# Kernel optimization log

Hardware: AMD Instinct MI355X
Metric: run time of the kernel (lower is better)

Reference implementation:

```python
import jax, jax.numpy as jnp
import numpy as np

B, H, W, C = 32, 512, 512, 3
OUT_H, OUT_W = 224, 224


def setup_inputs() -> dict:
    key = jax.random.key(0)
    k1, k2 = jax.random.split(key)
    images = jax.random.uniform(k1, (B, H, W, C), dtype=jnp.float32)
    identity = jnp.array([[1.0, 0.0, 0.0], [0.0, 1.0, 0.0]], dtype=jnp.float32)
    matrices = identity[None] + 0.05 * jax.random.normal(k2, (B, 2, 3), dtype=jnp.float32)
    return {"images": images, "matrices": matrices}


def _affine_warp(image, M):
    # image: (H, W, C); M: (2, 3) mapping output pixel (y, x, 1) -> source (y, x).
    h, w, _ = image.shape
    dt = image.dtype
    ys, xs = jnp.meshgrid(jnp.arange(h, dtype=dt), jnp.arange(w, dtype=dt), indexing="ij")
    src_y = M[0, 0] * ys + M[0, 1] * xs + M[0, 2]
    src_x = M[1, 0] * ys + M[1, 1] * xs + M[1, 2]
    y0 = jnp.floor(src_y)
    x0 = jnp.floor(src_x)
    wy = (src_y - y0)[..., None]
    wx = (src_x - x0)[..., None]
    y0i = y0.astype(jnp.int32)
    x0i = x0.astype(jnp.int32)

    def gather(yi, xi):
        valid = (yi >= 0) & (yi < h) & (xi >= 0) & (xi < w)
        yc = jnp.clip(yi, 0, h - 1)
        xc = jnp.clip(xi, 0, w - 1)
        return image[yc, xc] * valid[..., None].astype(dt)  # zero fill outside

    v00 = gather(y0i, x0i)
    v01 = gather(y0i, x0i + 1)
    v10 = gather(y0i + 1, x0i)
    v11 = gather(y0i + 1, x0i + 1)
    top = v00 * (1.0 - wx) + v01 * wx
    bot = v10 * (1.0 - wx) + v11 * wx
    return top * (1.0 - wy) + bot * wy


def reference(images, matrices):
    # batch_transform: per-sample affine warp (bilinear sampling, zero padding)
    warped = jax.vmap(_affine_warp)(images, matrices)  # (B, H, W, C)
    # batch_resize: bilinear resize to the layer's target shape
    b, _, _, c = warped.shape
    return jax.image.resize(warped, (b, OUT_H, OUT_W, c), method="bilinear")
```

## Files before the change

kernel.cpp:

```cpp
#include <hip/hip_runtime.h>
#include <hip/hip_bf16.h>
#include <math.h>

constexpr int B  = 32;
constexpr int H  = 512;
constexpr int W  = 512;
constexpr int OH = 224;
constexpr int OW = 224;

constexpr int TILE = 16;
constexpr int WIN  = 40;
constexpr int NT   = OH / TILE;
constexpr int NB   = B * NT * NT;
constexpr int THREADS = 256;

__global__ __launch_bounds__(THREADS, 8) void warp_resize_tiled(const float* __restrict__ img,
                                                                const float* __restrict__ mats,
                                                                float* __restrict__ out) {
    __shared__ __hip_bfloat16 sWp[3][WIN][WIN];
    __shared__ float          sV[TILE][WIN * 3];

    int bid = (int)blockIdx.x;
    bid = (bid & 7) * (NB / 8) + (bid >> 3);

    const int b   = bid / (NT * NT);
    const int rm  = bid % (NT * NT);
    const int ty  = rm / NT;
    const int tx  = rm % NT;
    const int tid = (int)threadIdx.x;

    const float* Mp = mats + b * 6;
    const float m00 = Mp[0], m01 = Mp[1], m02 = Mp[2];
    const float m10 = Mp[3], m11 = Mp[4], m12 = Mp[5];

    const float s     = 512.0f / 224.0f;
    const float invks = 224.0f / 512.0f;

    const int oy_base = ty * TILE;
    const int ox_base = tx * TILE;
    const int jy0 = (int)ceilf((oy_base + 0.5f) * s - 0.5f - s);
    const int jx0 = (int)ceilf((ox_base + 0.5f) * s - 0.5f - s);

    const float* imgb = img + (size_t)b * H * W * 3;

    const float y_lo = (float)jy0, y_hi = (float)(jy0 + WIN - 1);
    const float x_lo = (float)jx0, x_hi = (float)(jx0 + WIN - 1);
    const float cy00 = m00 * y_lo + m01 * x_lo + m02;
    const float cy01 = m00 * y_lo + m01 * x_hi + m02;
    const float cy10 = m00 * y_hi + m01 * x_lo + m02;
    const float cy11 = m00 * y_hi + m01 * x_hi + m02;
    const float cx00 = m10 * y_lo + m11 * x_lo + m12;
    const float cx01 = m10 * y_lo + m11 * x_hi + m12;
    const float cx10 = m10 * y_hi + m11 * x_lo + m12;
    const float cx11 = m10 * y_hi + m11 * x_hi + m12;
    const float miny = fminf(fminf(cy00, cy01), fminf(cy10, cy11));
    const float maxy = fmaxf(fmaxf(cy00, cy01), fmaxf(cy10, cy11));
    const float minx = fminf(fminf(cx00, cx01), fminf(cx10, cx11));
    const float maxx = fmaxf(fmaxf(cx00, cx01), fmaxf(cx10, cx11));
    const bool interior = (miny >= 0.01f) && (maxy <= 510.9f) &&
                          (minx >= 0.01f) && (maxx <= 510.9f);

    if (interior) {
        for (int e = tid; e < WIN * WIN; e += THREADS) {
            const int r = e / WIN;
            const int c = e - r * WIN;
            const float yf = (float)(jy0 + r);
            const float xf = (float)(jx0 + c);
            const float src_y = m00 * yf + m01 * xf + m02;
            const float src_x = m10 * yf + m11 * xf + m12;
            const float fy0 = floorf(src_y);
            const float fx0 = floorf(src_x);
            const float fy  = src_y - fy0;
            const float fx  = src_x - fx0;
            const int off = ((int)fy0 * W + (int)fx0) * 3;
            const float* p0 = imgb + off;
            const float* p1 = p0 + W * 3;
            const float a0 = p0[0], a1 = p0[1], a2 = p0[2];
            const float a3 = p0[3], a4 = p0[4], a5 = p0[5];
            const float b0 = p1[0], b1 = p1[1], b2 = p1[2];
            const float b3 = p1[3], b4 = p1[4], b5 = p1[5];
            const float w00 = (1.0f - fy) * (1.0f - fx);
            const float w01 = (1.0f - fy) * fx;
            const float w10 = fy * (1.0f - fx);
            const float w11 = fy * fx;
            sWp[0][r][c] = __float2bfloat16(a0 * w00 + a3 * w01 + b0 * w10 + b3 * w11);
            sWp[1][r][c] = __float2bfloat16(a1 * w00 + a4 * w01 + b1 * w10 + b4 * w11);
            sWp[2][r][c] = __float2bfloat16(a2 * w00 + a5 * w01 + b2 * w10 + b5 * w11);
        }
    } else {
        for (int e = tid; e < WIN * WIN; e += THREADS) {
            const int r = e / WIN;
            const int c = e - r * WIN;
            const float yf = (float)(jy0 + r);
            const float xf = (float)(jx0 + c);
            const float src_y = m00 * yf + m01 * xf + m02;
            const float src_x = m10 * yf + m11 * xf + m12;
            const float fy0 = floorf(src_y);
            const float fx0 = floorf(src_x);
            const float fy  = src_y - fy0;
            const float fx  = src_x - fx0;
            const int iy0 = (int)fy0;
            const int ix0 = (int)fx0;
            float v[4][3];
#pragma unroll
            for (int t = 0; t < 4; ++t) {
                const int yi = iy0 + (t >> 1);
                const int xi = ix0 + (t & 1);
                if (yi >= 0 && yi < H && xi >= 0 && xi < W) {
                    const float* p = imgb + (yi * W + xi) * 3;
                    v[t][0] = p[0]; v[t][1] = p[1]; v[t][2] = p[2];
                } else {
                    v[t][0] = 0.0f; v[t][1] = 0.0f; v[t][2] = 0.0f;
                }
            }
            const float w00 = (1.0f - fy) * (1.0f - fx);
            const float w01 = (1.0f - fy) * fx;
            const float w10 = fy * (1.0f - fx);
            const float w11 = fy * fx;
            sWp[0][r][c] = __float2bfloat16(v[0][0] * w00 + v[1][0] * w01 + v[2][0] * w10 + v[3][0] * w11);
            sWp[1][r][c] = __float2bfloat16(v[0][1] * w00 + v[1][1] * w01 + v[2][1] * w10 + v[3][1] * w11);
            sWp[2][r][c] = __float2bfloat16(v[0][2] * w00 + v[1][2] * w01 + v[2][2] * w10 + v[3][2] * w11);
        }
    }
    __syncthreads();

    for (int e = tid; e < TILE * WIN; e += THREADS) {
        const int r = e / WIN;
        const int c = e - r * WIN;
        const int oy = oy_base + r;
        const float sfy = (oy + 0.5f) * s - 0.5f;
        const int j0 = (int)ceilf(sfy - s);
        float wk[5];
        float sum = 0.0f;
#pragma unroll
        for (int k = 0; k < 5; ++k) {
            const int jy = j0 + k;
            float wv = 1.0f - fabsf(sfy - (float)jy) * invks;
            wv = (jy >= 0 && jy < H) ? fmaxf(wv, 0.0f) : 0.0f;
            wk[k] = wv; sum += wv;
        }
        const float inv = 1.0f / sum;
        float a0 = 0.0f, a1 = 0.0f, a2 = 0.0f;
#pragma unroll
        for (int k = 0; k < 5; ++k) {
            const int rr = j0 + k - jy0;
            const float wv = wk[k];
            a0 += wv * __bfloat162float(sWp[0][rr][c]);
            a1 += wv * __bfloat162float(sWp[1][rr][c]);
            a2 += wv * __bfloat162float(sWp[2][rr][c]);
        }
        sV[r][c * 3 + 0] = a0 * inv;
        sV[r][c * 3 + 1] = a1 * inv;
        sV[r][c * 3 + 2] = a2 * inv;
    }
    __syncthreads();

    {
        const int oxl = tid % TILE;
        const int oyl = tid / TILE;
        const int ox  = ox_base + oxl;
        const int oy  = oy_base + oyl;
        const float sfx = (ox + 0.5f) * s - 0.5f;
        const int j0 = (int)ceilf(sfx - s);
        float wk[5];
        float sum = 0.0f;
#pragma unroll
        for (int k = 0; k < 5; ++k) {
            const int jx = j0 + k;
            float wv = 1.0f - fabsf(sfx - (float)jx) * invks;
            wv = (jx >= 0 && jx < W) ? fmaxf(wv, 0.0f) : 0.0f;
            wk[k] = wv; sum += wv;
        }
        const float inv = 1.0f / sum;
        float a0 = 0.0f, a1 = 0.0f, a2 = 0.0f;
#pragma unroll
        for (int k = 0; k < 5; ++k) {
            const int cc = j0 + k - jx0;
            const float wv = wk[k];
            a0 += wv * sV[oyl][cc * 3 + 0];
            a1 += wv * sV[oyl][cc * 3 + 1];
            a2 += wv * sV[oyl][cc * 3 + 2];
        }
        float* o = out + (((size_t)b * OH + oy) * OW + ox) * 3;
        o[0] = a0 * inv;
        o[1] = a1 * inv;
        o[2] = a2 * inv;
    }
}

extern "C" void kernel_launch(void* const* d_in, const int* in_sizes, int n_in,
                              void* d_out, int out_size, void* d_ws, size_t ws_size,
                              hipStream_t stream) {
    const float* img  = (const float*)d_in[0];
    const float* mats = (const float*)d_in[1];
    float*       out  = (float*)d_out;

    hipLaunchKernelGGL(warp_resize_tiled, dim3(NB), dim3(THREADS), 0, stream, img, mats, out);
}
```

Baseline: 161.1 us.

## Pack bf16 channels into uint2 in shared memory and precompute resize weights

Stores the three warped channels per pixel as packed bf16 in a single uint2 shared-memory entry, so one 8-byte LDS replaces three separate 2-byte loads. The intermediate vertical-pass buffer also becomes packed bf16 instead of fp32. Per-row and per-column resize weights are computed once by 32 threads into shared tables with normalization folded in, instead of being recomputed in every inner loop. This cuts LDS instruction count and ALU work, but adds another bf16 rounding step on the intermediate, which reduces accuracy.

```diff
diff --git a/kernel.cpp b/kernel.cpp
--- a/kernel.cpp
+++ b/kernel.cpp
@@ -14,11 +14,26 @@
 constexpr int NB   = B * NT * NT;
 constexpr int THREADS = 256;
 
+union BfPack { __hip_bfloat162 h; unsigned u; };
+
+static __device__ inline unsigned pack_bf2(float a, float b) {
+    BfPack p; p.h = __float22bfloat162_rn(make_float2(a, b));
+    return p.u;
+}
+static __device__ inline unsigned pack_bf1(float a) {
+    BfPack p; p.h = __float22bfloat162_rn(make_float2(a, 0.0f));
+    return p.u;
+}
+static __device__ inline float lo_bf(unsigned q) { return __uint_as_float(q << 16); }
+static __device__ inline float hi_bf(unsigned q) { return __uint_as_float(q & 0xffff0000u); }
+
 __global__ __launch_bounds__(THREADS, 8) void warp_resize_tiled(const float* __restrict__ img,
                                                                 const float* __restrict__ mats,
                                                                 float* __restrict__ out) {
-    __shared__ __hip_bfloat16 sWp[3][WIN][WIN];
-    __shared__ float          sV[TILE][WIN * 3];
+    __shared__ uint2 sW[WIN][WIN];
+    __shared__ uint2 sV[TILE][WIN];
+    __shared__ float wyt[TILE][5], wxt[TILE][5];
+    __shared__ int   jyt[TILE], jxt[TILE];
 
     int bid = (int)blockIdx.x;
     bid = (bid & 7) * (NB / 8) + (bid >> 3);
@@ -42,6 +57,33 @@
     const int jx0 = (int)ceilf((ox_base + 0.5f) * s - 0.5f - s);
 
     const float* imgb = img + (size_t)b * H * W * 3;
+
+    if (tid < 2 * TILE) {
+        const bool isx = tid >= TILE;
+        const int  i   = isx ? tid - TILE : tid;
+        const int  ob  = isx ? ox_base : oy_base;
+        const int  jw0 = isx ? jx0 : jy0;
+        const float sf = ((float)(ob + i) + 0.5f) * s - 0.5f;
+        const int  j0 = (int)ceilf(sf - s);
+        float w[5]; float sum = 0.0f;
+#pragma unroll
+        for (int k = 0; k < 5; ++k) {
+            const int j = j0 + k;
+            float wv = 1.0f - fabsf(sf - (float)j) * invks;
+            wv = (j >= 0 && j < H) ? fmaxf(wv, 0.0f) : 0.0f;
+            w[k] = wv; sum += wv;
+        }
+        const float inv = 1.0f / sum;
+        if (isx) {
+            jxt[i] = j0 - jw0;
+#pragma unroll
+            for (int k = 0; k < 5; ++k) wxt[i][k] = w[k] * inv;
+        } else {
+            jyt[i] = j0 - jw0;
+#pragma unroll
+            for (int k = 0; k < 5; ++k) wyt[i][k] = w[k] * inv;
+        }
+    }
 
     const float y_lo = (float)jy0, y_hi = (float)(jy0 + WIN - 1);
     const float x_lo = (float)jx0, x_hi = (float)(jx0 + WIN - 1);
@@ -83,9 +125,11 @@
             const float w01 = (1.0f - fy) * fx;
             const float w10 = fy * (1.0f - fx);
             const float w11 = fy * fx;
-            sWp[0][r][c] = __float2bfloat16(a0 * w00 + a3 * w01 + b0 * w10 + b3 * w11);
-            sWp[1][r][c] = __float2bfloat16(a1 * w00 + a4 * w01 + b1 * w10 + b4 * w11);
-            sWp[2][r][c] = __float2bfloat16(a2 * w00 + a5 * w01 + b2 * w10 + b5 * w11);
+            const float c0 = a0 * w00 + a3 * w01 + b0 * w10 + b3 * w11;
+            const float c1 = a1 * w00 + a4 * w01 + b1 * w10 + b4 * w11;
+            const float c2 = a2 * w00 + a5 * w01 + b2 * w10 + b5 * w11;
+            uint2 q; q.x = pack_bf2(c0, c1); q.y = pack_bf1(c2);
+            sW[r][c] = q;
         }
     } else {
         for (int e = tid; e < WIN * WIN; e += THREADS) {
@@ -117,9 +161,11 @@
             const float w01 = (1.0f - fy) * fx;
             const float w10 = fy * (1.0f - fx);
             const float w11 = fy * fx;
-            sWp[0][r][c] = __float2bfloat16(v[0][0] * w00 + v[1][0] * w01 + v[2][0] * w10 + v[3][0] * w11);
-            sWp[1][r][c] = __float2bfloat16(v[0][1] * w00 + v[1][1] * w01 + v[2][1] * w10 + v[3][1] * w11);
-            sWp[2][r][c] = __float2bfloat16(v[0][2] * w00 + v[1][2] * w01 + v[2][2] * w10 + v[3][2] * w11);
+            const float c0 = v[0][0] * w00 + v[1][0] * w01 + v[2][0] * w10 + v[3][0] * w11;
+            const float c1 = v[0][1] * w00 + v[1][1] * w01 + v[2][1] * w10 + v[3][1] * w11;
+            const float c2 = v[0][2] * w00 + v[1][2] * w01 + v[2][2] * w10 + v[3][2] * w11;
+            uint2 q; q.x = pack_bf2(c0, c1); q.y = pack_bf1(c2);
+            sW[r][c] = q;
         }
     }
     __syncthreads();
@@ -127,64 +173,40 @@
     for (int e = tid; e < TILE * WIN; e += THREADS) {
         const int r = e / WIN;
         const int c = e - r * WIN;
-        const int oy = oy_base + r;
-        const float sfy = (oy + 0.5f) * s - 0.5f;
-        const int j0 = (int)ceilf(sfy - s);
-        float wk[5];
-        float sum = 0.0f;
+        const int rr0 = jyt[r];
+        float a0 = 0.0f, a1 = 0.0f, a2 = 0.0f;
 #pragma unroll
         for (int k = 0; k < 5; ++k) {
-            const int jy = j0 + k;
-            float wv = 1.0f - fabsf(sfy - (float)jy) * invks;
-            wv = (jy >= 0 && jy < H) ? fmaxf(wv, 0.0f) : 0.0f;
-            wk[k] = wv; sum += wv;
-        }
-        const float inv = 1.0f / sum;
+            const uint2 q = sW[rr0 + k][c];
+            const float wv = wyt[r][k];
+            a0 += wv * lo_bf(q.x);
+            a1 += wv * hi_bf(q.x);
+            a2 += wv * lo_bf(q.y);
+        }
+        uint2 q; q.x = pack_bf2(a0, a1); q.y = pack_bf1(a2);
+        sV[r][c] = q;
+    }
+    __syncthreads();
+
+    {
+        const int oxl = tid & (TILE - 1);
+        const int oyl = tid >> 4;
+        const int cc0 = jxt[oxl];
         float a0 = 0.0f, a1 = 0.0f, a2 = 0.0f;
 #pragma unroll
         for (int k = 0; k < 5; ++k) {
-            const int rr = j0 + k - jy0;
-            const float wv = wk[k];
-            a0 += wv * __bfloat162float(sWp[0][rr][c]);
-            a1 += wv * __bfloat162float(sWp[1][rr][c]);
-            a2 += wv * __bfloat162float(sWp[2][rr][c]);
-        }
-        sV[r][c * 3 + 0] = a0 * inv;
-        sV[r][c * 3 + 1] = a1 * inv;
-        sV[r][c * 3 + 2] = a2 * inv;
-    }
-    __syncthreads();
-
-    {
-        const int oxl = tid % TILE;
-        const int oyl = tid / TILE;
-        const int ox  = ox_base + oxl;
-        const int oy  = oy_base + oyl;
-        const float sfx = (ox + 0.5f) * s - 0.5f;
-        const int j0 = (int)ceilf(sfx - s);
-        float wk[5];
-        float sum = 0.0f;
-#pragma unroll
-        for (int k = 0; k < 5; ++k) {
-            const int jx = j0 + k;
-            float wv = 1.0f - fabsf(sfx - (float)jx) * invks;
-            wv = (jx >= 0 && jx < W) ? fmaxf(wv, 0.0f) : 0.0f;
-            wk[k] = wv; sum += wv;
-        }
-        const float inv = 1.0f / sum;
-        float a0 = 0.0f, a1 = 0.0f, a2 = 0.0f;
-#pragma unroll
-        for (int k = 0; k < 5; ++k) {
-            const int cc = j0 + k - jx0;
-            const float wv = wk[k];
-            a0 += wv * sV[oyl][cc * 3 + 0];
-            a1 += wv * sV[oyl][cc * 3 + 1];
-            a2 += wv * sV[oyl][cc * 3 + 2];
-        }
+            const uint2 q = sV[oyl][cc0 + k];
+            const float wv = wxt[oxl][k];
+            a0 += wv * lo_bf(q.x);
+            a1 += wv * hi_bf(q.x);
+            a2 += wv * lo_bf(q.y);
+        }
+        const int ox = ox_base + oxl;
+        const int oy = oy_base + oyl;
         float* o = out + (((size_t)b * OH + oy) * OW + ox) * 3;
-        o[0] = a0 * inv;
-        o[1] = a1 * inv;
-        o[2] = a2 * inv;
+        o[0] = a0;
+        o[1] = a1;
+        o[2] = a2;
     }
 }
 
```

After: 158.4 us. About the same (-1.7%).
